# Kernel tuning notes

Measured on AMD Instinct MI355X. Metric: run time of the kernel, lower is better.

## Reference

```python
import jax, jax.numpy as jnp
import numpy as np

N = 4096      # nodes
F = 512       # input_dim
D = 512       # output_dim
H = 8         # n_heads
d = D // H    # per-head out_sz


def setup_inputs() -> dict:
    key = jax.random.key(0)
    ks = jax.random.split(key, 6)
    x = jax.random.normal(ks[0], (N, F), dtype=jnp.float32)
    adj = (jax.random.uniform(ks[1], (N, N)) < 0.01).astype(jnp.float32)
    adj = jnp.maximum(adj, jnp.eye(N, dtype=jnp.float32))
    # per-head params: weight transform W, attention vectors a1/a2 (conv1d k=1 -> dot) with biases
    W = jax.random.normal(ks[2], (H, F, d), dtype=jnp.float32) * 0.05
    a1 = jax.random.normal(ks[3], (H, d), dtype=jnp.float32) * 0.05
    a2 = jax.random.normal(ks[4], (H, d), dtype=jnp.float32) * 0.05
    b1 = jnp.zeros((H,), dtype=jnp.float32)
    b2 = jnp.zeros((H,), dtype=jnp.float32)
    return {"x": x, "adj": adj, "W": W, "a1": a1, "b1": b1, "a2": a2, "b2": b2}


def reference(x, adj, W, a1, b1, a2, b2):
    # per-node linear transform for all heads: [H, N, d]
    seq_fts = jnp.einsum('nf,hfd->hnd', x, W)
    # attention logits components (conv1d(out=1,k=1) == dot + bias): [H, N]
    f1 = jnp.einsum('hnd,hd->hn', seq_fts, a1) + b1[:, None]
    f2 = jnp.einsum('hnd,hd->hn', seq_fts, a2) + b2[:, None]
    # logits = adj * f1_i + adj * f2_j  (adj acts multiplicatively AND as sparsity mask)
    logits = adj[None, :, :] * f1[:, :, None] + adj[None, :, :] * f2[:, None, :]
    lrelu = jnp.maximum(0.2 * logits, logits)  # leaky_relu alpha=0.2
    # sparse softmax over adjacency nonzeros (tf.sparse_softmax over from_dense pattern)
    mask = adj != 0
    scores = jnp.where(mask[None, :, :], lrelu, -jnp.inf)
    coefs = jax.nn.softmax(scores, axis=-1)           # [H, N, N], zero off-mask
    vals = jnp.einsum('hnm,hmd->hnd', coefs, seq_fts)  # sparse-dense matmul per head
    # concat heads on feature axis, batch dim of 1, elu activation
    h = jnp.transpose(vals, (1, 0, 2)).reshape(N, H * d)[None, :, :]
    return jax.nn.elu(h)
```

## Files before the change

kernel.cpp:

```cpp
#include <hip/hip_runtime.h>
#include <math.h>

#define N_NODES 4096
#define F_DIM   512
#define D_DIM   512
#define H_HEADS 8
#define HD      64
#define CAP     160

typedef __attribute__((ext_vector_type(8))) short short8;
typedef __attribute__((ext_vector_type(4))) float f32x4;

__device__ __forceinline__ unsigned short f2bf(float f) {
    unsigned int u = __builtin_bit_cast(unsigned int, f);
    return (unsigned short)((u + 0x7FFFu + ((u >> 16) & 1u)) >> 16);
}
__device__ __forceinline__ float bflo(unsigned int u) {
    return __builtin_bit_cast(float, u << 16);
}
__device__ __forceinline__ float bfhi(unsigned int u) {
    return __builtin_bit_cast(float, u & 0xffff0000u);
}

__global__ __launch_bounds__(256) void prep(const float* __restrict__ adj,
                                            const float* __restrict__ x,
                                            const float* __restrict__ W,
                                            unsigned short* __restrict__ xb,
                                            unsigned short* __restrict__ Bt,
                                            int* __restrict__ rowIdx,
                                            int* __restrict__ cntArr) {
    const int b = blockIdx.x;
    if (b < 1024) {
        const int lane = threadIdx.x & 63;
        const int w    = threadIdx.x >> 6;
        const int r    = b * 4 + w;
        const float* arow = adj + (size_t)r * N_NODES;

        f32x4 vq[16];
        #pragma unroll
        for (int q = 0; q < 16; ++q)
            vq[q] = *(const f32x4*)&arow[q * 256 + lane * 4];

        unsigned long long mask = 0ull;
        #pragma unroll
        for (int q = 0; q < 16; ++q) {
            if (vq[q].x != 0.0f) mask |= 1ull << (q * 4 + 0);
            if (vq[q].y != 0.0f) mask |= 1ull << (q * 4 + 1);
            if (vq[q].z != 0.0f) mask |= 1ull << (q * 4 + 2);
            if (vq[q].w != 0.0f) mask |= 1ull << (q * 4 + 3);
        }
        const int n_t = __popcll(mask);
        int incl = n_t;
        #pragma unroll
        for (int off = 1; off < 64; off <<= 1) {
            int u = __shfl_up(incl, off, 64);
            if (lane >= off) incl += u;
        }
        const int tot = __shfl(incl, 63, 64);
        int pos = incl - n_t;
        const int rbase = r * CAP;
        while (mask) {
            const int bit = __builtin_ctzll(mask);
            mask &= mask - 1;
            const int col = ((bit >> 2) << 8) + (lane << 2) + (bit & 3);
            if (pos < CAP) rowIdx[rbase + pos] = col;
            ++pos;
        }
        if (lane == 0) cntArr[r] = tot;
    } else if (b < 2048) {
        const int t = (b - 1024) * 256 + threadIdx.x;
        const float4 v0 = *(const float4*)&x[t * 8];
        const float4 v1 = *(const float4*)&x[t * 8 + 4];
        unsigned short o[8] = {f2bf(v0.x), f2bf(v0.y), f2bf(v0.z), f2bf(v0.w),
                               f2bf(v1.x), f2bf(v1.y), f2bf(v1.z), f2bf(v1.w)};
        *(uint4*)&xb[t * 8] = *(const uint4*)o;
    } else {
        const int t = (b - 2048) * 256 + threadIdx.x;
        const int n = t >> 6;
        const int kb = (t & 63) * 8;
        const int h = n >> 6, dd = n & 63;
        const float* src = W + (size_t)h * F_DIM * HD + dd;
        unsigned short o[8];
        #pragma unroll
        for (int q = 0; q < 8; ++q) o[q] = f2bf(src[(size_t)(kb + q) * HD]);
        *(uint4*)&Bt[(size_t)n * F_DIM + kb] = *(const uint4*)o;
    }
}

__global__ __launch_bounds__(256) void gemm_mfma(const unsigned short* __restrict__ A,
                                                 const unsigned short* __restrict__ Bt,
                                                 const float* __restrict__ a1,
                                                 const float* __restrict__ b1,
                                                 const float* __restrict__ a2,
                                                 const float* __restrict__ b2,
                                                 unsigned short* __restrict__ seqb,
                                                 float* __restrict__ f1t,
                                                 float* __restrict__ f2t) {
    __shared__ unsigned short As[64][40];
    __shared__ unsigned short Bs[64][40];
    __shared__ float sF[2][64][2];

    const int tid  = threadIdx.x;
    const int lane = tid & 63;
    const int w    = tid >> 6;
    const int wr   = w >> 1, wc = w & 1;
    const int i0   = blockIdx.x * 64;
    const int h    = blockIdx.y;
    const int n0   = h * 64;

    const int ar = tid >> 2;
    const int ac = (tid & 3) * 8;

    const int rlane = lane & 15;
    const int q     = lane >> 4;
    const int klane = q * 8;

    f32x4 acc[2][2] = {};

    for (int k0 = 0; k0 < F_DIM; k0 += 32) {
        const uint4 av = *(const uint4*)&A[(size_t)(i0 + ar) * F_DIM + k0 + ac];
        const uint4 bv = *(const uint4*)&Bt[(size_t)(n0 + ar) * F_DIM + k0 + ac];
        __syncthreads();
        *(uint4*)&As[ar][ac] = av;
        *(uint4*)&Bs[ar][ac] = bv;
        __syncthreads();

        short8 a_frag[2], b_frag[2];
        #pragma unroll
        for (int mi = 0; mi < 2; ++mi)
            a_frag[mi] = *(const short8*)&As[wr * 32 + mi * 16 + rlane][klane];
        #pragma unroll
        for (int ni = 0; ni < 2; ++ni)
            b_frag[ni] = *(const short8*)&Bs[wc * 32 + ni * 16 + rlane][klane];
        #pragma unroll
        for (int mi = 0; mi < 2; ++mi)
            #pragma unroll
            for (int ni = 0; ni < 2; ++ni)
                acc[mi][ni] = __builtin_amdgcn_mfma_f32_16x16x32_bf16(
                    a_frag[mi], b_frag[ni], acc[mi][ni], 0, 0, 0);
    }

    #pragma unroll
    for (int mi = 0; mi < 2; ++mi)
        #pragma unroll
        for (int ni = 0; ni < 2; ++ni)
            #pragma unroll
            for (int r = 0; r < 4; ++r) {
                const int row = i0 + wr * 32 + mi * 16 + q * 4 + r;
                const int col = n0 + wc * 32 + ni * 16 + rlane;
                seqb[(size_t)row * D_DIM + col] = f2bf(acc[mi][ni][r]);
            }

    float a1v[2], a2v[2];
    #pragma unroll
    for (int ni = 0; ni < 2; ++ni) {
        const int c = wc * 32 + ni * 16 + rlane;
        a1v[ni] = a1[h * HD + c];
        a2v[ni] = a2[h * HD + c];
    }
    #pragma unroll
    for (int mi = 0; mi < 2; ++mi)
        #pragma unroll
        for (int r = 0; r < 4; ++r) {
            float s1 = acc[mi][0][r] * a1v[0] + acc[mi][1][r] * a1v[1];
            float s2 = acc[mi][0][r] * a2v[0] + acc[mi][1][r] * a2v[1];
            #pragma unroll
            for (int m = 1; m < 16; m <<= 1) {
                s1 += __shfl_xor(s1, m, 64);
                s2 += __shfl_xor(s2, m, 64);
            }
            if (rlane == 0) {
                const int rl = wr * 32 + mi * 16 + q * 4 + r;
                sF[0][rl][wc] = s1;
                sF[1][rl][wc] = s2;
            }
        }
    __syncthreads();
    if (tid < 64) {
        const int row = i0 + tid;
        f1t[row * 8 + h] = sF[0][tid][0] + sF[0][tid][1] + b1[h];
        f2t[row * 8 + h] = sF[1][tid][0] + sF[1][tid][1] + b2[h];
    }
}

__global__ __launch_bounds__(128) void attn(const float* __restrict__ adj,
                                            const unsigned short* __restrict__ seqb,
                                            const float* __restrict__ f1t,
                                            const float* __restrict__ f2t,
                                            const int* __restrict__ rowIdx,
                                            const int* __restrict__ cntArr,
                                            float* __restrict__ out) {
    __shared__ int   sIdx[CAP];
    __shared__ float sP[CAP][8];
    __shared__ float sRed[2][8];
    __shared__ float sAcc[64][8];

    const int i    = blockIdx.x;
    const int tid  = threadIdx.x;
    const int lane = tid & 63;
    const int w    = tid >> 6;

    const int cnt = cntArr[i];
    if (cnt <= CAP) {
        for (int jj = tid; jj < cnt; jj += 128)
            sIdx[jj] = rowIdx[i * CAP + jj];
    }
    __syncthreads();

    const float4 f1a = *(const float4*)&f1t[i * 8];
    const float4 f1b = *(const float4*)&f1t[i * 8 + 4];
    const float f1r[8] = {f1a.x, f1a.y, f1a.z, f1a.w, f1b.x, f1b.y, f1b.z, f1b.w};

    const int h8 = lane >> 3;
    float acc[8] = {0.f, 0.f, 0.f, 0.f, 0.f, 0.f, 0.f, 0.f};
    float myinv;

    if (cnt <= CAP) {
        float m[8];
        #pragma unroll
        for (int h = 0; h < 8; ++h) m[h] = -INFINITY;
        for (int jj = tid; jj < cnt; jj += 128) {
            const int j = sIdx[jj];
            const float4 fa = *(const float4*)&f2t[j * 8];
            const float4 fb = *(const float4*)&f2t[j * 8 + 4];
            const float f2r[8] = {fa.x, fa.y, fa.z, fa.w, fb.x, fb.y, fb.z, fb.w};
            float L[8];
            #pragma unroll
            for (int h = 0; h < 8; ++h) {
                float v = f1r[h] + f2r[h];
                v = fmaxf(v, 0.2f * v);
                L[h] = v;
                m[h] = fmaxf(m[h], v);
            }
            f32x4 La = {L[0], L[1], L[2], L[3]};
            f32x4 Lb = {L[4], L[5], L[6], L[7]};
            *(f32x4*)&sP[jj][0] = La;
            *(f32x4*)&sP[jj][4] = Lb;
        }
        #pragma unroll
        for (int off = 32; off; off >>= 1)
            #pragma unroll
            for (int h = 0; h < 8; ++h)
                m[h] = fmaxf(m[h], __shfl_xor(m[h], off, 64));
        if (lane == 0) {
            f32x4 ma = {m[0], m[1], m[2], m[3]};
            f32x4 mb = {m[4], m[5], m[6], m[7]};
            *(f32x4*)&sRed[w][0] = ma;
            *(f32x4*)&sRed[w][4] = mb;
        }
        __syncthreads();
        #pragma unroll
        for (int h = 0; h < 8; ++h) m[h] = fmaxf(sRed[0][h], sRed[1][h]);
        __syncthreads();

        float s[8] = {0.f, 0.f, 0.f, 0.f, 0.f, 0.f, 0.f, 0.f};
        for (int jj = tid; jj < cnt; jj += 128) {
            const f32x4 La = *(const f32x4*)&sP[jj][0];
            const f32x4 Lb = *(const f32x4*)&sP[jj][4];
            const float L[8] = {La.x, La.y, La.z, La.w, Lb.x, Lb.y, Lb.z, Lb.w};
            float e[8];
            #pragma unroll
            for (int h = 0; h < 8; ++h) {
                e[h] = __expf(L[h] - m[h]);
                s[h] += e[h];
            }
            f32x4 ea = {e[0], e[1], e[2], e[3]};
            f32x4 eb = {e[4], e[5], e[6], e[7]};
            *(f32x4*)&sP[jj][0] = ea;
            *(f32x4*)&sP[jj][4] = eb;
        }
        #pragma unroll
        for (int off = 32; off; off >>= 1)
            #pragma unroll
            for (int h = 0; h < 8; ++h)
                s[h] += __shfl_xor(s[h], off, 64);
        if (lane == 0) {
            f32x4 sa = {s[0], s[1], s[2], s[3]};
            f32x4 sb = {s[4], s[5], s[6], s[7]};
            *(f32x4*)&sRed[w][0] = sa;
            *(f32x4*)&sRed[w][4] = sb;
        }
        __syncthreads();
        myinv = 1.0f / (sRed[0][h8] + sRed[1][h8]);

        const int cnt2 = (cnt + 1) >> 1;
        const int jlo = w ? cnt2 : 0;
        const int jhi = w ? cnt  : cnt2;
        const char* __restrict__ vbase = (const char*)seqb + lane * 16;
        int jj = jlo;
        for (; jj + 4 <= jhi; jj += 4) {
            const int4 j4 = *(const int4*)&sIdx[jj];
            const float p0 = sP[jj + 0][h8];
            const float p1 = sP[jj + 1][h8];
            const float p2 = sP[jj + 2][h8];
            const float p3 = sP[jj + 3][h8];
            const uint4 u0 = *(const uint4*)(vbase + ((size_t)j4.x << 10));
            const uint4 u1 = *(const uint4*)(vbase + ((size_t)j4.y << 10));
            const uint4 u2 = *(const uint4*)(vbase + ((size_t)j4.z << 10));
            const uint4 u3 = *(const uint4*)(vbase + ((size_t)j4.w << 10));
            const unsigned int w0[4] = {u0.x, u0.y, u0.z, u0.w};
            const unsigned int w1[4] = {u1.x, u1.y, u1.z, u1.w};
            const unsigned int w2[4] = {u2.x, u2.y, u2.z, u2.w};
            const unsigned int w3[4] = {u3.x, u3.y, u3.z, u3.w};
            #pragma unroll
            for (int k = 0; k < 4; ++k) {
                acc[k * 2 + 0] = fmaf(p0, bflo(w0[k]), acc[k * 2 + 0]);
                acc[k * 2 + 1] = fmaf(p0, bfhi(w0[k]), acc[k * 2 + 1]);
                acc[k * 2 + 0] = fmaf(p1, bflo(w1[k]), acc[k * 2 + 0]);
                acc[k * 2 + 1] = fmaf(p1, bfhi(w1[k]), acc[k * 2 + 1]);
                acc[k * 2 + 0] = fmaf(p2, bflo(w2[k]), acc[k * 2 + 0]);
                acc[k * 2 + 1] = fmaf(p2, bfhi(w2[k]), acc[k * 2 + 1]);
                acc[k * 2 + 0] = fmaf(p3, bflo(w3[k]), acc[k * 2 + 0]);
                acc[k * 2 + 1] = fmaf(p3, bfhi(w3[k]), acc[k * 2 + 1]);
            }
        }
        for (; jj < jhi; ++jj) {
            const int j = sIdx[jj];
            const float p = sP[jj][h8];
            const uint4 u = *(const uint4*)(vbase + ((size_t)j << 10));
            const unsigned int wv[4] = {u.x, u.y, u.z, u.w};
            #pragma unroll
            for (int k = 0; k < 4; ++k) {
                acc[k * 2 + 0] = fmaf(p, bflo(wv[k]), acc[k * 2 + 0]);
                acc[k * 2 + 1] = fmaf(p, bfhi(wv[k]), acc[k * 2 + 1]);
            }
        }
    } else {
        const float* arow = adj + (size_t)i * N_NODES;
        float m[8];
        #pragma unroll
        for (int h = 0; h < 8; ++h) m[h] = -INFINITY;
        for (int j = tid; j < N_NODES; j += 128) {
            if (arow[j] != 0.0f) {
                const float4 fa = *(const float4*)&f2t[j * 8];
                const float4 fb = *(const float4*)&f2t[j * 8 + 4];
                const float f2r[8] = {fa.x, fa.y, fa.z, fa.w, fb.x, fb.y, fb.z, fb.w};
                #pragma unroll
                for (int h = 0; h < 8; ++h) {
                    float v = f1r[h] + f2r[h];
                    v = fmaxf(v, 0.2f * v);
                    m[h] = fmaxf(m[h], v);
                }
            }
        }
        #pragma unroll
        for (int off = 32; off; off >>= 1)
            #pragma unroll
            for (int h = 0; h < 8; ++h)
                m[h] = fmaxf(m[h], __shfl_xor(m[h], off, 64));
        if (lane == 0) {
            f32x4 ma = {m[0], m[1], m[2], m[3]};
            f32x4 mb = {m[4], m[5], m[6], m[7]};
            *(f32x4*)&sRed[w][0] = ma;
            *(f32x4*)&sRed[w][4] = mb;
        }
        __syncthreads();
        #pragma unroll
        for (int h = 0; h < 8; ++h) m[h] = fmaxf(sRed[0][h], sRed[1][h]);
        __syncthreads();

        float s[8] = {0.f, 0.f, 0.f, 0.f, 0.f, 0.f, 0.f, 0.f};
        for (int j = tid; j < N_NODES; j += 128) {
            if (arow[j] != 0.0f) {
                const float4 fa = *(const float4*)&f2t[j * 8];
                const float4 fb = *(const float4*)&f2t[j * 8 + 4];
                const float f2r[8] = {fa.x, fa.y, fa.z, fa.w, fb.x, fb.y, fb.z, fb.w};
                #pragma unroll
                for (int h = 0; h < 8; ++h) {
                    float v = f1r[h] + f2r[h];
                    v = fmaxf(v, 0.2f * v);
                    s[h] += __expf(v - m[h]);
                }
            }
        }
        #pragma unroll
        for (int off = 32; off; off >>= 1)
            #pragma unroll
            for (int h = 0; h < 8; ++h)
                s[h] += __shfl_xor(s[h], off, 64);
        if (lane == 0) {
            f32x4 sa = {s[0], s[1], s[2], s[3]};
            f32x4 sb = {s[4], s[5], s[6], s[7]};
            *(f32x4*)&sRed[w][0] = sa;
            *(f32x4*)&sRed[w][4] = sb;
        }
        __syncthreads();
        myinv = 1.0f / (sRed[0][h8] + sRed[1][h8]);
        const float mh = m[h8], f1h = f1r[h8];

        const char* __restrict__ vbase = (const char*)seqb + lane * 16;
        const int jlo = w * (N_NODES / 2), jhi = jlo + N_NODES / 2;
        for (int j = jlo; j < jhi; ++j) {
            if (arow[j] != 0.0f) {
                float v = f1h + f2t[j * 8 + h8];
                v = fmaxf(v, 0.2f * v);
                const float p = __expf(v - mh);
                const uint4 u = *(const uint4*)(vbase + ((size_t)j << 10));
                const unsigned int wv[4] = {u.x, u.y, u.z, u.w};
                #pragma unroll
                for (int k = 0; k < 4; ++k) {
                    acc[k * 2 + 0] = fmaf(p, bflo(wv[k]), acc[k * 2 + 0]);
                    acc[k * 2 + 1] = fmaf(p, bfhi(wv[k]), acc[k * 2 + 1]);
                }
            }
        }
    }

    if (w == 1) {
        f32x4 pa = {acc[0], acc[1], acc[2], acc[3]};
        f32x4 pb = {acc[4], acc[5], acc[6], acc[7]};
        *(f32x4*)&sAcc[lane][0] = pa;
        *(f32x4*)&sAcc[lane][4] = pb;
    }
    __syncthreads();
    if (w == 0) {
        float o[8];
        #pragma unroll
        for (int k = 0; k < 8; ++k) {
            const float v = (acc[k] + sAcc[lane][k]) * myinv;
            o[k] = (v > 0.f) ? v : expm1f(v);
        }
        f32x4 oa = {o[0], o[1], o[2], o[3]};
        f32x4 ob = {o[4], o[5], o[6], o[7]};
        float* dst = &out[(size_t)i * D_DIM + lane * 8];
        __builtin_nontemporal_store(oa, (f32x4*)dst);
        __builtin_nontemporal_store(ob, (f32x4*)(dst + 4));
    }
}

extern "C" void kernel_launch(void* const* d_in, const int* in_sizes, int n_in,
                              void* d_out, int out_size, void* d_ws, size_t ws_size,
                              hipStream_t stream) {
    const float* x   = (const float*)d_in[0];
    const float* adj = (const float*)d_in[1];
    const float* W   = (const float*)d_in[2];
    const float* a1  = (const float*)d_in[3];
    const float* b1  = (const float*)d_in[4];
    const float* a2  = (const float*)d_in[5];
    const float* b2  = (const float*)d_in[6];
    float* out = (float*)d_out;

    char* ws = (char*)d_ws;
    unsigned short* seqb = (unsigned short*)ws;
    unsigned short* xb   = (unsigned short*)(ws + (size_t)N_NODES * D_DIM * 2);
    unsigned short* Bt   = (unsigned short*)(ws + (size_t)N_NODES * D_DIM * 4);
    float* f1t = (float*)(ws + (size_t)N_NODES * D_DIM * 4 + (size_t)D_DIM * F_DIM * 2);
    float* f2t = f1t + (size_t)N_NODES * H_HEADS;
    int* rowIdx = (int*)(f2t + (size_t)N_NODES * H_HEADS);
    int* cntArr = rowIdx + (size_t)N_NODES * CAP;

    prep<<<2176, 256, 0, stream>>>(adj, x, W, xb, Bt, rowIdx, cntArr);

    dim3 gg(N_NODES / 64, D_DIM / 64);
    gemm_mfma<<<gg, 256, 0, stream>>>(xb, Bt, a1, b1, a2, b2, seqb, f1t, f2t);

    attn<<<N_NODES, 128, 0, stream>>>(adj, seqb, f1t, f2t, rowIdx, cntArr, out);
}
```

Baseline: 48.15 us.

## Overlap adjacency compaction with GEMM and keep attention logits in registers

Adjacency-row compaction moves out of the prep kernel into extra blocks of the GEMM launch, so the bandwidth-bound scan of adj runs at the same time as the compute-bound MFMA GEMM. Column indices shrink to 16-bit and use nontemporal stores and loads. In the attention kernel the per-neighbour logits now stay in registers (at most two per thread) instead of going through shared memory, one barrier is removed by using separate reduction buffers, and the gather loop is unrolled by 8. Costs are higher register pressure and a dependence on CAP being at most 256 for the two-slot scheme.

```diff
diff --git a/kernel.cpp b/kernel.cpp
--- a/kernel.cpp
+++ b/kernel.cpp
@@ -22,60 +22,19 @@
     return __builtin_bit_cast(float, u & 0xffff0000u);
 }
 
-__global__ __launch_bounds__(256) void prep(const float* __restrict__ adj,
-                                            const float* __restrict__ x,
-                                            const float* __restrict__ W,
-                                            unsigned short* __restrict__ xb,
-                                            unsigned short* __restrict__ Bt,
-                                            int* __restrict__ rowIdx,
-                                            int* __restrict__ cntArr) {
-    const int b = blockIdx.x;
-    if (b < 1024) {
-        const int lane = threadIdx.x & 63;
-        const int w    = threadIdx.x >> 6;
-        const int r    = b * 4 + w;
-        const float* arow = adj + (size_t)r * N_NODES;
-
-        f32x4 vq[16];
-        #pragma unroll
-        for (int q = 0; q < 16; ++q)
-            vq[q] = *(const f32x4*)&arow[q * 256 + lane * 4];
-
-        unsigned long long mask = 0ull;
-        #pragma unroll
-        for (int q = 0; q < 16; ++q) {
-            if (vq[q].x != 0.0f) mask |= 1ull << (q * 4 + 0);
-            if (vq[q].y != 0.0f) mask |= 1ull << (q * 4 + 1);
-            if (vq[q].z != 0.0f) mask |= 1ull << (q * 4 + 2);
-            if (vq[q].w != 0.0f) mask |= 1ull << (q * 4 + 3);
-        }
-        const int n_t = __popcll(mask);
-        int incl = n_t;
-        #pragma unroll
-        for (int off = 1; off < 64; off <<= 1) {
-            int u = __shfl_up(incl, off, 64);
-            if (lane >= off) incl += u;
-        }
-        const int tot = __shfl(incl, 63, 64);
-        int pos = incl - n_t;
-        const int rbase = r * CAP;
-        while (mask) {
-            const int bit = __builtin_ctzll(mask);
-            mask &= mask - 1;
-            const int col = ((bit >> 2) << 8) + (lane << 2) + (bit & 3);
-            if (pos < CAP) rowIdx[rbase + pos] = col;
-            ++pos;
-        }
-        if (lane == 0) cntArr[r] = tot;
-    } else if (b < 2048) {
-        const int t = (b - 1024) * 256 + threadIdx.x;
+__global__ __launch_bounds__(256) void conv_inputs(const float* __restrict__ x,
+                                                   const float* __restrict__ W,
+                                                   unsigned short* __restrict__ xb,
+                                                   unsigned short* __restrict__ Bt) {
+    if (blockIdx.x < 1024) {
+        const int t = blockIdx.x * 256 + threadIdx.x;
         const float4 v0 = *(const float4*)&x[t * 8];
         const float4 v1 = *(const float4*)&x[t * 8 + 4];
         unsigned short o[8] = {f2bf(v0.x), f2bf(v0.y), f2bf(v0.z), f2bf(v0.w),
                                f2bf(v1.x), f2bf(v1.y), f2bf(v1.z), f2bf(v1.w)};
         *(uint4*)&xb[t * 8] = *(const uint4*)o;
     } else {
-        const int t = (b - 2048) * 256 + threadIdx.x;
+        const int t = (blockIdx.x - 1024) * 256 + threadIdx.x;
         const int n = t >> 6;
         const int kb = (t & 63) * 8;
         const int h = n >> 6, dd = n & 63;
@@ -87,15 +46,18 @@
     }
 }
 
-__global__ __launch_bounds__(256) void gemm_mfma(const unsigned short* __restrict__ A,
+__global__ __launch_bounds__(256) void gemm_plus(const unsigned short* __restrict__ A,
                                                  const unsigned short* __restrict__ Bt,
+                                                 const float* __restrict__ adj,
                                                  const float* __restrict__ a1,
                                                  const float* __restrict__ b1,
                                                  const float* __restrict__ a2,
                                                  const float* __restrict__ b2,
                                                  unsigned short* __restrict__ seqb,
                                                  float* __restrict__ f1t,
-                                                 float* __restrict__ f2t) {
+                                                 float* __restrict__ f2t,
+                                                 unsigned short* __restrict__ rowIdx,
+                                                 int* __restrict__ cntArr) {
     __shared__ unsigned short As[64][40];
     __shared__ unsigned short Bs[64][40];
     __shared__ float sF[2][64][2];
@@ -103,9 +65,49 @@
     const int tid  = threadIdx.x;
     const int lane = tid & 63;
     const int w    = tid >> 6;
+
+    if (blockIdx.x >= 512) {
+        const int r = (blockIdx.x - 512) * 4 + w;
+        const float* arow = adj + (size_t)r * N_NODES;
+
+        f32x4 vq[16];
+        #pragma unroll
+        for (int q = 0; q < 16; ++q)
+            vq[q] = *(const f32x4*)&arow[q * 256 + lane * 4];
+
+        unsigned long long mask = 0ull;
+        #pragma unroll
+        for (int q = 0; q < 16; ++q) {
+            if (vq[q].x != 0.0f) mask |= 1ull << (q * 4 + 0);
+            if (vq[q].y != 0.0f) mask |= 1ull << (q * 4 + 1);
+            if (vq[q].z != 0.0f) mask |= 1ull << (q * 4 + 2);
+            if (vq[q].w != 0.0f) mask |= 1ull << (q * 4 + 3);
+        }
+        const int n_t = __popcll(mask);
+        int incl = n_t;
+        #pragma unroll
+        for (int off = 1; off < 64; off <<= 1) {
+            int u = __shfl_up(incl, off, 64);
+            if (lane >= off) incl += u;
+        }
+        const int tot = __shfl(incl, 63, 64);
+        int pos = incl - n_t;
+        unsigned short* rbase = rowIdx + (size_t)r * CAP;
+        while (mask) {
+            const int bit = __builtin_ctzll(mask);
+            mask &= mask - 1;
+            const int col = ((bit >> 2) << 8) + (lane << 2) + (bit & 3);
+            if (pos < CAP)
+                __builtin_nontemporal_store((unsigned short)col, rbase + pos);
+            ++pos;
+        }
+        if (lane == 0) cntArr[r] = tot;
+        return;
+    }
+
     const int wr   = w >> 1, wc = w & 1;
-    const int i0   = blockIdx.x * 64;
-    const int h    = blockIdx.y;
+    const int i0   = (blockIdx.x & 63) * 64;
+    const int h    = blockIdx.x >> 6;
     const int n0   = h * 64;
 
     const int ar = tid >> 2;
@@ -187,12 +189,13 @@
                                             const unsigned short* __restrict__ seqb,
                                             const float* __restrict__ f1t,
                                             const float* __restrict__ f2t,
-                                            const int* __restrict__ rowIdx,
+                                            const unsigned short* __restrict__ rowIdx,
                                             const int* __restrict__ cntArr,
                                             float* __restrict__ out) {
     __shared__ int   sIdx[CAP];
     __shared__ float sP[CAP][8];
-    __shared__ float sRed[2][8];
+    __shared__ float sRedM[2][8];
+    __shared__ float sRedS[2][8];
     __shared__ float sAcc[64][8];
 
     const int i    = blockIdx.x;
@@ -202,8 +205,9 @@
 
     const int cnt = cntArr[i];
     if (cnt <= CAP) {
+        const unsigned short* rb = rowIdx + (size_t)i * CAP;
         for (int jj = tid; jj < cnt; jj += 128)
-            sIdx[jj] = rowIdx[i * CAP + jj];
+            sIdx[jj] = __builtin_nontemporal_load(rb + jj);
     }
     __syncthreads();
 
@@ -216,26 +220,37 @@
     float myinv;
 
     if (cnt <= CAP) {
+        const bool has0 = tid < cnt;
+        const bool has1 = tid + 128 < cnt;
+        float L0[8], L1[8];
         float m[8];
         #pragma unroll
         for (int h = 0; h < 8; ++h) m[h] = -INFINITY;
-        for (int jj = tid; jj < cnt; jj += 128) {
-            const int j = sIdx[jj];
+        if (has0) {
+            const int j = sIdx[tid];
             const float4 fa = *(const float4*)&f2t[j * 8];
             const float4 fb = *(const float4*)&f2t[j * 8 + 4];
             const float f2r[8] = {fa.x, fa.y, fa.z, fa.w, fb.x, fb.y, fb.z, fb.w};
-            float L[8];
             #pragma unroll
             for (int h = 0; h < 8; ++h) {
                 float v = f1r[h] + f2r[h];
                 v = fmaxf(v, 0.2f * v);
-                L[h] = v;
+                L0[h] = v;
                 m[h] = fmaxf(m[h], v);
             }
-            f32x4 La = {L[0], L[1], L[2], L[3]};
-            f32x4 Lb = {L[4], L[5], L[6], L[7]};
-            *(f32x4*)&sP[jj][0] = La;
-            *(f32x4*)&sP[jj][4] = Lb;
+        }
+        if (has1) {
+            const int j = sIdx[tid + 128];
+            const float4 fa = *(const float4*)&f2t[j * 8];
+            const float4 fb = *(const float4*)&f2t[j * 8 + 4];
+            const float f2r[8] = {fa.x, fa.y, fa.z, fa.w, fb.x, fb.y, fb.z, fb.w};
+            #pragma unroll
+            for (int h = 0; h < 8; ++h) {
+                float v = f1r[h] + f2r[h];
+                v = fmaxf(v, 0.2f * v);
+                L1[h] = v;
+                m[h] = fmaxf(m[h], v);
+            }
         }
         #pragma unroll
         for (int off = 32; off; off >>= 1)
@@ -245,29 +260,37 @@
         if (lane == 0) {
             f32x4 ma = {m[0], m[1], m[2], m[3]};
             f32x4 mb = {m[4], m[5], m[6], m[7]};
-            *(f32x4*)&sRed[w][0] = ma;
-            *(f32x4*)&sRed[w][4] = mb;
-        }
-        __syncthreads();
-        #pragma unroll
-        for (int h = 0; h < 8; ++h) m[h] = fmaxf(sRed[0][h], sRed[1][h]);
-        __syncthreads();
+            *(f32x4*)&sRedM[w][0] = ma;
+            *(f32x4*)&sRedM[w][4] = mb;
+        }
+        __syncthreads();
+        #pragma unroll
+        for (int h = 0; h < 8; ++h) m[h] = fmaxf(sRedM[0][h], sRedM[1][h]);
 
         float s[8] = {0.f, 0.f, 0.f, 0.f, 0.f, 0.f, 0.f, 0.f};
-        for (int jj = tid; jj < cnt; jj += 128) {
-            const f32x4 La = *(const f32x4*)&sP[jj][0];
-            const f32x4 Lb = *(const f32x4*)&sP[jj][4];
-            const float L[8] = {La.x, La.y, La.z, La.w, Lb.x, Lb.y, Lb.z, Lb.w};
+        if (has0) {
             float e[8];
             #pragma unroll
             for (int h = 0; h < 8; ++h) {
-                e[h] = __expf(L[h] - m[h]);
+                e[h] = __expf(L0[h] - m[h]);
                 s[h] += e[h];
             }
             f32x4 ea = {e[0], e[1], e[2], e[3]};
             f32x4 eb = {e[4], e[5], e[6], e[7]};
-            *(f32x4*)&sP[jj][0] = ea;
-            *(f32x4*)&sP[jj][4] = eb;
+            *(f32x4*)&sP[tid][0] = ea;
+            *(f32x4*)&sP[tid][4] = eb;
+        }
+        if (has1) {
+            float e[8];
+            #pragma unroll
+            for (int h = 0; h < 8; ++h) {
+                e[h] = __expf(L1[h] - m[h]);
+                s[h] += e[h];
+            }
+            f32x4 ea = {e[0], e[1], e[2], e[3]};
+            f32x4 eb = {e[4], e[5], e[6], e[7]};
+            *(f32x4*)&sP[tid + 128][0] = ea;
+            *(f32x4*)&sP[tid + 128][4] = eb;
         }
         #pragma unroll
         for (int off = 32; off; off >>= 1)
@@ -277,41 +300,44 @@
         if (lane == 0) {
             f32x4 sa = {s[0], s[1], s[2], s[3]};
             f32x4 sb = {s[4], s[5], s[6], s[7]};
-            *(f32x4*)&sRed[w][0] = sa;
-            *(f32x4*)&sRed[w][4] = sb;
-        }
-        __syncthreads();
-        myinv = 1.0f / (sRed[0][h8] + sRed[1][h8]);
+            *(f32x4*)&sRedS[w][0] = sa;
+            *(f32x4*)&sRedS[w][4] = sb;
+        }
+        __syncthreads();
+        myinv = 1.0f / (sRedS[0][h8] + sRedS[1][h8]);
 
         const int cnt2 = (cnt + 1) >> 1;
         const int jlo = w ? cnt2 : 0;
         const int jhi = w ? cnt  : cnt2;
         const char* __restrict__ vbase = (const char*)seqb + lane * 16;
         int jj = jlo;
-        for (; jj + 4 <= jhi; jj += 4) {
-            const int4 j4 = *(const int4*)&sIdx[jj];
-            const float p0 = sP[jj + 0][h8];
-            const float p1 = sP[jj + 1][h8];
-            const float p2 = sP[jj + 2][h8];
-            const float p3 = sP[jj + 3][h8];
-            const uint4 u0 = *(const uint4*)(vbase + ((size_t)j4.x << 10));
-            const uint4 u1 = *(const uint4*)(vbase + ((size_t)j4.y << 10));
-            const uint4 u2 = *(const uint4*)(vbase + ((size_t)j4.z << 10));
-            const uint4 u3 = *(const uint4*)(vbase + ((size_t)j4.w << 10));
-            const unsigned int w0[4] = {u0.x, u0.y, u0.z, u0.w};
-            const unsigned int w1[4] = {u1.x, u1.y, u1.z, u1.w};
-            const unsigned int w2[4] = {u2.x, u2.y, u2.z, u2.w};
-            const unsigned int w3[4] = {u3.x, u3.y, u3.z, u3.w};
-            #pragma unroll
-            for (int k = 0; k < 4; ++k) {
-                acc[k * 2 + 0] = fmaf(p0, bflo(w0[k]), acc[k * 2 + 0]);
-                acc[k * 2 + 1] = fmaf(p0, bfhi(w0[k]), acc[k * 2 + 1]);
-                acc[k * 2 + 0] = fmaf(p1, bflo(w1[k]), acc[k * 2 + 0]);
-                acc[k * 2 + 1] = fmaf(p1, bfhi(w1[k]), acc[k * 2 + 1]);
-                acc[k * 2 + 0] = fmaf(p2, bflo(w2[k]), acc[k * 2 + 0]);
-                acc[k * 2 + 1] = fmaf(p2, bfhi(w2[k]), acc[k * 2 + 1]);
-                acc[k * 2 + 0] = fmaf(p3, bflo(w3[k]), acc[k * 2 + 0]);
-                acc[k * 2 + 1] = fmaf(p3, bfhi(w3[k]), acc[k * 2 + 1]);
+        for (; jj + 8 <= jhi; jj += 8) {
+            #pragma unroll
+            for (int u2 = 0; u2 < 2; ++u2) {
+                const int4 j4 = *(const int4*)&sIdx[jj + u2 * 4];
+                const float p0 = sP[jj + u2 * 4 + 0][h8];
+                const float p1 = sP[jj + u2 * 4 + 1][h8];
+                const float p2 = sP[jj + u2 * 4 + 2][h8];
+                const float p3 = sP[jj + u2 * 4 + 3][h8];
+                const uint4 u0 = *(const uint4*)(vbase + ((size_t)j4.x << 10));
+                const uint4 u1 = *(const uint4*)(vbase + ((size_t)j4.y << 10));
+                const uint4 u2v = *(const uint4*)(vbase + ((size_t)j4.z << 10));
+                const uint4 u3 = *(const uint4*)(vbase + ((size_t)j4.w << 10));
+                const unsigned int w0[4] = {u0.x, u0.y, u0.z, u0.w};
+                const unsigned int w1[4] = {u1.x, u1.y, u1.z, u1.w};
+                const unsigned int w2[4] = {u2v.x, u2v.y, u2v.z, u2v.w};
+                const unsigned int w3[4] = {u3.x, u3.y, u3.z, u3.w};
+                #pragma unroll
+                for (int k = 0; k < 4; ++k) {
+                    acc[k * 2 + 0] = fmaf(p0, bflo(w0[k]), acc[k * 2 + 0]);
+                    acc[k * 2 + 1] = fmaf(p0, bfhi(w0[k]), acc[k * 2 + 1]);
+                    acc[k * 2 + 0] = fmaf(p1, bflo(w1[k]), acc[k * 2 + 0]);
+                    acc[k * 2 + 1] = fmaf(p1, bfhi(w1[k]), acc[k * 2 + 1]);
+                    acc[k * 2 + 0] = fmaf(p2, bflo(w2[k]), acc[k * 2 + 0]);
+                    acc[k * 2 + 1] = fmaf(p2, bfhi(w2[k]), acc[k * 2 + 1]);
+                    acc[k * 2 + 0] = fmaf(p3, bflo(w3[k]), acc[k * 2 + 0]);
+                    acc[k * 2 + 1] = fmaf(p3, bfhi(w3[k]), acc[k * 2 + 1]);
+                }
             }
         }
         for (; jj < jhi; ++jj) {
@@ -351,13 +377,12 @@
         if (lane == 0) {
             f32x4 ma = {m[0], m[1], m[2], m[3]};
             f32x4 mb = {m[4], m[5], m[6], m[7]};
-            *(f32x4*)&sRed[w][0] = ma;
-            *(f32x4*)&sRed[w][4] = mb;
-        }
-        __syncthreads();
-        #pragma unroll
-        for (int h = 0; h < 8; ++h) m[h] = fmaxf(sRed[0][h], sRed[1][h]);
-        __syncthreads();
+            *(f32x4*)&sRedM[w][0] = ma;
+            *(f32x4*)&sRedM[w][4] = mb;
+        }
+        __syncthreads();
+        #pragma unroll
+        for (int h = 0; h < 8; ++h) m[h] = fmaxf(sRedM[0][h], sRedM[1][h]);
 
         float s[8] = {0.f, 0.f, 0.f, 0.f, 0.f, 0.f, 0.f, 0.f};
         for (int j = tid; j < N_NODES; j += 128) {
@@ -381,11 +406,11 @@
         if (lane == 0) {
             f32x4 sa = {s[0], s[1], s[2], s[3]};
             f32x4 sb = {s[4], s[5], s[6], s[7]};
-            *(f32x4*)&sRed[w][0] = sa;
-            *(f32x4*)&sRed[w][4] = sb;
-        }
-        __syncthreads();
-        myinv = 1.0f / (sRed[0][h8] + sRed[1][h8]);
+            *(f32x4*)&sRedS[w][0] = sa;
+            *(f32x4*)&sRedS[w][4] = sb;
+        }
+        __syncthreads();
+        myinv = 1.0f / (sRedS[0][h8] + sRedS[1][h8]);
         const float mh = m[h8], f1h = f1r[h8];
 
         const char* __restrict__ vbase = (const char*)seqb + lane * 16;
@@ -446,13 +471,13 @@
     unsigned short* Bt   = (unsigned short*)(ws + (size_t)N_NODES * D_DIM * 4);
     float* f1t = (float*)(ws + (size_t)N_NODES * D_DIM * 4 + (size_t)D_DIM * F_DIM * 2);
     float* f2t = f1t + (size_t)N_NODES * H_HEADS;
-    int* rowIdx = (int*)(f2t + (size_t)N_NODES * H_HEADS);
-    int* cntArr = rowIdx + (size_t)N_NODES * CAP;
-
-    prep<<<2176, 256, 0, stream>>>(adj, x, W, xb, Bt, rowIdx, cntArr);
-
-    dim3 gg(N_NODES / 64, D_DIM / 64);
-    gemm_mfma<<<gg, 256, 0, stream>>>(xb, Bt, a1, b1, a2, b2, seqb, f1t, f2t);
+    unsigned short* rowIdx = (unsigned short*)(f2t + (size_t)N_NODES * H_HEADS);
+    int* cntArr = (int*)(rowIdx + (size_t)N_NODES * CAP);
+
+    conv_inputs<<<1152, 256, 0, stream>>>(x, W, xb, Bt);
+
+    gemm_plus<<<1536, 256, 0, stream>>>(xb, Bt, adj, a1, b1, a2, b2,
+                                        seqb, f1t, f2t, rowIdx, cntArr);
 
     attn<<<N_NODES, 128, 0, stream>>>(adj, seqb, f1t, f2t, rowIdx, cntArr, out);
 }
```

After: 48.50 us. Within noise of the previous version (+0.7%).
